# Kernel optimization log

Measured on AMD Instinct MI355X. Metric: run time of the kernel, lower is better.

Reference implementation:

```python
import jax, jax.numpy as jnp
import numpy as np

N, E, IN, OUT, EF = 20000, 100000, 32, 32, 16
NEG = -1e30  # finite sentinel for masked scores (avoids inf*0 grads)


def setup_inputs() -> dict:
    key = jax.random.key(0)
    ks = jax.random.split(key, 8)
    return {
        "feat": jax.random.normal(ks[0], (N, IN), jnp.float32),
        "efeat": jax.random.normal(ks[1], (E, EF), jnp.float32),
        "src": jax.random.randint(ks[2], (E,), 0, N, dtype=jnp.int32),
        "dst": jax.random.randint(ks[3], (E,), 0, N, dtype=jnp.int32),
        "etype": jax.random.randint(ks[4], (E,), 0, 2, dtype=jnp.int32),
        "attn_w": jax.random.normal(ks[5], (2 * IN, 1), jnp.float32) * 0.1,
        "attn_b": jnp.zeros((1,), jnp.float32),
        "ef1_w": jax.random.normal(ks[6], (EF, IN * OUT), jnp.float32) * 0.05,
        "ef1_b": jnp.zeros((IN * OUT,), jnp.float32),
        "ef2_w": jax.random.normal(ks[7], (EF, IN * OUT), jnp.float32) * 0.05,
        "ef2_b": jnp.zeros((IN * OUT,), jnp.float32),
        "bias": jnp.zeros((OUT,), jnp.float32),
    }


def reference(feat, efeat, src, dst, etype, attn_w, attn_b,
              ef1_w, ef1_b, ef2_w, ef2_b, bias):
    n_nodes = feat.shape[0]
    z_src = feat[src]                      # [E, IN] gather src features
    z_dst = feat[dst]                      # [E, IN] gather dst features
    # per-edge scalar attention score: leaky_relu(Linear(cat(z_src, z_dst)))
    score = jax.nn.leaky_relu(
        (jnp.concatenate([z_src, z_dst], axis=1) @ attn_w + attn_b)[:, 0]
    )  # [E]

    def relation_agg(mask, w, b):
        # edge-specific weight matrices: [E, IN, OUT]
        We = (efeat @ w + b).reshape(E, IN, OUT)
        # message per edge = src_feat @ W_e  (sum over IN commutes with attn)
        msg = jnp.einsum('ei,eio->eo', z_src, We)        # [E, OUT]
        # segment softmax over incoming edges of this relation per dst node
        s = jnp.where(mask, score, NEG)
        smax = jax.ops.segment_max(s, dst, num_segments=n_nodes)
        ex = jnp.where(mask, jnp.exp(s - smax[dst]), 0.0)
        den = jax.ops.segment_sum(ex, dst, num_segments=n_nodes)
        alpha = ex / jnp.where(den > 0, den, 1.0)[dst]   # [E]
        # attention-weighted scatter-sum to dst nodes
        return jax.ops.segment_sum(alpha[:, None] * msg, dst,
                                   num_segments=n_nodes)  # [N, OUT]

    rst = relation_agg(etype == 0, ef1_w, ef1_b) \
        + relation_agg(etype == 1, ef2_w, ef2_b) \
        + bias
    return rst
```

## Files before the change

kernel.cpp:

```cpp
#include <hip/hip_runtime.h>

typedef __attribute__((ext_vector_type(8))) short bf16x8;
typedef __attribute__((ext_vector_type(16))) float f32x16;

__device__ __forceinline__ unsigned short f2b(float x) {
    unsigned u = __float_as_uint(x);
    unsigned r = (u + 0x7fffu + ((u >> 16) & 1u)) >> 16;
    return (unsigned short)r;
}

__global__ void k_init(const float* __restrict__ feat, const float* __restrict__ attn_w,
                       const int* __restrict__ dst, const int* __restrict__ etype,
                       const float* __restrict__ w1, const float* __restrict__ b1,
                       const float* __restrict__ w2, const float* __restrict__ b2,
                       float* __restrict__ ps, float* __restrict__ pd,
                       unsigned short* __restrict__ PA, int* __restrict__ hist,
                       int E, int N) {
    int idx = blockIdx.x * blockDim.x + threadIdx.x;
    if (idx < N) {
        const float4* zp = (const float4*)(feat + (long)idx * 32);
        const float4* aw = (const float4*)attn_w;
        float a = 0.f, b = 0.f;
        #pragma unroll
        for (int j = 0; j < 8; ++j) {
            float4 z = zp[j], wa = aw[j], wb = aw[8 + j];
            a = fmaf(z.x, wa.x, a); a = fmaf(z.y, wa.y, a);
            a = fmaf(z.z, wa.z, a); a = fmaf(z.w, wa.w, a);
            b = fmaf(z.x, wb.x, b); b = fmaf(z.y, wb.y, b);
            b = fmaf(z.z, wb.z, b); b = fmaf(z.w, wb.w, b);
        }
        ps[idx] = a; pd[idx] = b;
    }
    if (idx < 2 * 17 * 2 * 64) {
        int l = idx & 63;
        int x = idx >> 6;
        int h = x & 1; x >>= 1;
        int t = x % 17;
        int r = x / 17;
        const float* W = r ? w2 : w1;
        const float* B = r ? b2 : b1;
        int o = l & 31;
        int kb = h * 16 + (l >> 5) * 8;
        unsigned short v[8];
        #pragma unroll
        for (int j = 0; j < 8; ++j) {
            int i = kb + j;
            float s = (t < 16) ? W[t * 1024 + i * 32 + o] : B[i * 32 + o];
            v[j] = f2b(s);
        }
        uint4 pack;
        pack.x = (unsigned)v[0] | ((unsigned)v[1] << 16);
        pack.y = (unsigned)v[2] | ((unsigned)v[3] << 16);
        pack.z = (unsigned)v[4] | ((unsigned)v[5] << 16);
        pack.w = (unsigned)v[6] | ((unsigned)v[7] << 16);
        *((uint4*)PA + idx) = pack;
    }
    if (idx < E) atomicAdd(&hist[etype[idx] * N + dst[idx]], 1);
}

__global__ __launch_bounds__(256) void k_scan1(const int* __restrict__ hist,
                                               int* __restrict__ rowptr,
                                               int* __restrict__ bsum, int n) {
    __shared__ int s[256];
    int t = threadIdx.x;
    int i0 = blockIdx.x * 1024 + t * 4;
    int h[4];
    #pragma unroll
    for (int j = 0; j < 4; ++j) h[j] = (i0 + j < n) ? hist[i0 + j] : 0;
    int tot = h[0] + h[1] + h[2] + h[3];
    s[t] = tot;
    __syncthreads();
    for (int d = 1; d < 256; d <<= 1) {
        int x = (t >= d) ? s[t - d] : 0;
        __syncthreads();
        s[t] += x;
        __syncthreads();
    }
    int excl = s[t] - tot;
    int run = excl;
    #pragma unroll
    for (int j = 0; j < 4; ++j) {
        if (i0 + j < n) rowptr[i0 + j] = run;
        run += h[j];
    }
    if (t == 255) bsum[blockIdx.x] = s[255];
}

__global__ void k_scan2(int* __restrict__ bsum, int nb) {
    int lane = threadIdx.x & 63;
    int carry = 0;
    for (int c = 0; c < nb; c += 64) {
        int i = c + lane;
        int v = (i < nb) ? bsum[i] : 0;
        int inc = v;
        #pragma unroll
        for (int d = 1; d < 64; d <<= 1) {
            int x = __shfl_up(inc, d);
            if (lane >= d) inc += x;
        }
        if (i < nb) bsum[i] = inc - v + carry;
        carry += __shfl(inc, 63);
    }
}

__global__ void k_scan3(int* __restrict__ rowptr, const int* __restrict__ bsum,
                        int* __restrict__ cursor, int n, int E) {
    int i = blockIdx.x * blockDim.x + threadIdx.x;
    if (i < n) {
        int v = rowptr[i] + bsum[i >> 10];
        rowptr[i] = v;
        cursor[i] = v;
    }
    if (i == 0) rowptr[n] = E;
}

__global__ void k_score(const int* __restrict__ src, const int* __restrict__ dst,
                        const int* __restrict__ etype,
                        const float* __restrict__ ps, const float* __restrict__ pd,
                        const float* __restrict__ attn_b,
                        int* __restrict__ cursor, int* __restrict__ sortidx,
                        float* __restrict__ exs, int E, int N) {
    int e = blockIdx.x * blockDim.x + threadIdx.x;
    if (e >= E) return;
    int d = dst[e];
    float sc = ps[src[e]] + pd[d] + attn_b[0];
    sc = sc >= 0.f ? sc : 0.01f * sc;
    float v = __expf(sc);
    int key = etype[e] * N + d;
    int pos = atomicAdd(&cursor[key], 1);
    sortidx[pos] = e;
    exs[pos] = v;
}

__global__ __launch_bounds__(256) void k_msg(
    const float* __restrict__ feat, const float* __restrict__ efeat,
    const int* __restrict__ src, const unsigned short* __restrict__ PA,
    const int* __restrict__ sortidx, const int* __restrict__ rowptr,
    float* __restrict__ wmsg, int E, int N) {
    int r = blockIdx.y;
    int cnt0 = rowptr[N];
    int relstart = r ? cnt0 : 0;
    int count = r ? (E - cnt0) : cnt0;
    int base = blockIdx.x * 128;
    if (count <= 0 || base >= count) return;

    __shared__ __align__(16) char smem[18432];
    unsigned short (*z_bf)[32] = (unsigned short(*)[32])smem;
    float (*ut)[128] = (float(*)[128])(smem + 8192);
    float (*msgl)[36] = (float(*)[36])smem;

    int tid = threadIdx.x;
    {
        int el = tid >> 1, half = tid & 1;
        int gi = base + el;
        int e = sortidx[relstart + min(gi, count - 1)];
        int s = src[e];
        const float4* zp = (const float4*)(feat + (long)s * 32 + half * 16);
        float4 a0 = zp[0], a1 = zp[1], a2 = zp[2], a3 = zp[3];
        unsigned short* zd = &z_bf[el][half * 16];
        zd[0] = f2b(a0.x); zd[1] = f2b(a0.y); zd[2]  = f2b(a0.z); zd[3]  = f2b(a0.w);
        zd[4] = f2b(a1.x); zd[5] = f2b(a1.y); zd[6]  = f2b(a1.z); zd[7]  = f2b(a1.w);
        zd[8] = f2b(a2.x); zd[9] = f2b(a2.y); zd[10] = f2b(a2.z); zd[11] = f2b(a2.w);
        zd[12] = f2b(a3.x); zd[13] = f2b(a3.y); zd[14] = f2b(a3.z); zd[15] = f2b(a3.w);
        const float4* up = (const float4*)(efeat + (long)e * 16 + half * 8);
        float4 c0 = up[0], c1 = up[1];
        int fb = half * 8;
        ut[fb + 0][el] = c0.x; ut[fb + 1][el] = c0.y;
        ut[fb + 2][el] = c0.z; ut[fb + 3][el] = c0.w;
        ut[fb + 4][el] = c1.x; ut[fb + 5][el] = c1.y;
        ut[fb + 6][el] = c1.z; ut[fb + 7][el] = c1.w;
    }
    __syncthreads();

    int lane = tid & 63;
    int ecol = (tid >> 6) * 32 + (lane & 31);
    int kb = (lane >> 5) * 8;
    bf16x8 b0 = *(const bf16x8*)&z_bf[ecol][kb];
    bf16x8 b1 = *(const bf16x8*)&z_bf[ecol][16 + kb];

    const bf16x8* pa = (const bf16x8*)PA + (long)r * 34 * 64 + lane;

    f32x16 msg;
    {
        bf16x8 a0 = pa[32 * 64];
        bf16x8 a1 = pa[33 * 64];
        f32x16 c;
        #pragma unroll
        for (int k = 0; k < 16; ++k) c[k] = 0.f;
        c = __builtin_amdgcn_mfma_f32_32x32x16_bf16(a0, b0, c, 0, 0, 0);
        c = __builtin_amdgcn_mfma_f32_32x32x16_bf16(a1, b1, c, 0, 0, 0);
        msg = c;
    }
    float uu[16];
    #pragma unroll
    for (int t = 0; t < 16; ++t) uu[t] = ut[t][ecol];
    #pragma unroll 4
    for (int t = 0; t < 16; ++t) {
        bf16x8 a0 = pa[(t * 2 + 0) * 64];
        bf16x8 a1 = pa[(t * 2 + 1) * 64];
        f32x16 c;
        #pragma unroll
        for (int k = 0; k < 16; ++k) c[k] = 0.f;
        c = __builtin_amdgcn_mfma_f32_32x32x16_bf16(a0, b0, c, 0, 0, 0);
        c = __builtin_amdgcn_mfma_f32_32x32x16_bf16(a1, b1, c, 0, 0, 0);
        #pragma unroll
        for (int k = 0; k < 16; ++k) msg[k] = fmaf(uu[t], c[k], msg[k]);
    }
    __syncthreads();

    {
        int ob = 4 * (lane >> 5);
        #pragma unroll
        for (int k = 0; k < 16; ++k)
            msgl[ecol][ob + (k & 3) + 8 * (k >> 2)] = msg[k];
    }
    __syncthreads();

    {
        float4* wb = (float4*)(wmsg + (long)(relstart + base) * 32);
        #pragma unroll
        for (int j = 0; j < 4; ++j) {
            int flat = j * 256 + tid;
            int row = flat >> 3, col = (flat & 7) * 4;
            if (base + row < count)
                wb[flat] = *(const float4*)&msgl[row][col];
        }
    }
}

__global__ void k_reduce(const int* __restrict__ rowptr, const float* __restrict__ exs,
                         const float* __restrict__ wmsg, const float* __restrict__ bias,
                         float* __restrict__ out, int N) {
    int tid = blockIdx.x * blockDim.x + threadIdx.x;
    if (tid >= N * 8) return;
    int n = tid >> 3, og = tid & 7;
    float4 acc = ((const float4*)bias)[og];
    #pragma unroll 1
    for (int r = 0; r < 2; ++r) {
        int k = r * N + n;
        int s = rowptr[k], e2 = rowptr[k + 1];
        if (s >= e2) continue;
        float den = 0.f;
        #pragma unroll 1
        for (int p = s; p < e2; ++p) den += exs[p];
        float inv = 1.f / den;
        #pragma unroll 1
        for (int p = s; p < e2; ++p) {
            float w = exs[p] * inv;
            float4 m = *(const float4*)(wmsg + (long)p * 32 + og * 4);
            acc.x = fmaf(w, m.x, acc.x); acc.y = fmaf(w, m.y, acc.y);
            acc.z = fmaf(w, m.z, acc.z); acc.w = fmaf(w, m.w, acc.w);
        }
    }
    ((float4*)out)[tid] = acc;
}

extern "C" void kernel_launch(void* const* d_in, const int* in_sizes, int n_in,
                              void* d_out, int out_size, void* d_ws, size_t ws_size,
                              hipStream_t stream) {
    const float* feat   = (const float*)d_in[0];
    const float* efeat  = (const float*)d_in[1];
    const int*   src    = (const int*)d_in[2];
    const int*   dst    = (const int*)d_in[3];
    const int*   etype  = (const int*)d_in[4];
    const float* attn_w = (const float*)d_in[5];
    const float* attn_b = (const float*)d_in[6];
    const float* ef1_w  = (const float*)d_in[7];
    const float* ef1_b  = (const float*)d_in[8];
    const float* ef2_w  = (const float*)d_in[9];
    const float* ef2_b  = (const float*)d_in[10];
    const float* bias   = (const float*)d_in[11];

    int E = in_sizes[2];
    int N = in_sizes[0] / 32;
    int n2 = 2 * N;

    float*          ps      = (float*)d_ws;
    float*          pd      = ps + N;
    unsigned short* PA      = (unsigned short*)(pd + N);
    int*            hist    = (int*)(PA + 2 * 17 * 2 * 64 * 8);
    int*            rowptr  = hist + n2;
    int*            cursor  = rowptr + n2 + 1;
    int*            bsum    = cursor + n2;
    int*            sortidx = bsum + 64;
    float*          exs     = (float*)(sortidx + E);
    float*          wmsg    = (float*)(((size_t)(exs + E) + 15) & ~(size_t)15);
    float*          out     = (float*)d_out;

    int nb = (n2 + 1023) / 1024;

    hipMemsetAsync(hist, 0, (size_t)n2 * sizeof(int), stream);
    k_init<<<(E + 255) / 256, 256, 0, stream>>>(feat, attn_w, dst, etype,
                                                ef1_w, ef1_b, ef2_w, ef2_b,
                                                ps, pd, PA, hist, E, N);
    k_scan1<<<nb, 256, 0, stream>>>(hist, rowptr, bsum, n2);
    k_scan2<<<1, 64, 0, stream>>>(bsum, nb);
    k_scan3<<<(n2 + 255) / 256, 256, 0, stream>>>(rowptr, bsum, cursor, n2, E);
    k_score<<<(E + 255) / 256, 256, 0, stream>>>(src, dst, etype, ps, pd, attn_b,
                                                 cursor, sortidx, exs, E, N);
    dim3 mgrid((E + 127) / 128, 2);
    k_msg<<<mgrid, 256, 0, stream>>>(feat, efeat, src, PA, sortidx, rowptr,
                                     wmsg, E, N);
    k_reduce<<<(N * 8 + 255) / 256, 256, 0, stream>>>(rowptr, exs, wmsg, bias, out, N);
}
```

Baseline: 54.31 us.

## Fuse preprocessing kernels into one cooperative kernel and store messages in bf16

Replaces the memset plus five small preprocessing kernels (init, three scan passes, score/bucket) with one cooperative kernel using grid-wide syncs, cutting launch overhead and inter-kernel gaps. It also stores per-edge weighted messages in bf16 instead of fp32, halving the write and read traffic between the message and reduce kernels. Costs are grid-sync overhead, a fixed 256-block grid that may underuse the GPU for edge loops, and extra rounding of messages to bf16. The single-block bsum scan now assumes nb is at most 64.

```diff
diff --git a/kernel.cpp b/kernel.cpp
--- a/kernel.cpp
+++ b/kernel.cpp
@@ -1,4 +1,7 @@
 #include <hip/hip_runtime.h>
+#include <hip/hip_cooperative_groups.h>
+
+namespace cg = cooperative_groups;
 
 typedef __attribute__((ext_vector_type(8))) short bf16x8;
 typedef __attribute__((ext_vector_type(16))) float f32x16;
@@ -8,17 +11,34 @@
     unsigned r = (u + 0x7fffu + ((u >> 16) & 1u)) >> 16;
     return (unsigned short)r;
 }
-
-__global__ void k_init(const float* __restrict__ feat, const float* __restrict__ attn_w,
-                       const int* __restrict__ dst, const int* __restrict__ etype,
-                       const float* __restrict__ w1, const float* __restrict__ b1,
-                       const float* __restrict__ w2, const float* __restrict__ b2,
-                       float* __restrict__ ps, float* __restrict__ pd,
-                       unsigned short* __restrict__ PA, int* __restrict__ hist,
-                       int E, int N) {
-    int idx = blockIdx.x * blockDim.x + threadIdx.x;
-    if (idx < N) {
-        const float4* zp = (const float4*)(feat + (long)idx * 32);
+__device__ __forceinline__ float b2f(unsigned short u) {
+    return __uint_as_float((unsigned)u << 16);
+}
+
+__global__ __launch_bounds__(256) void k_pre(
+    const float* __restrict__ feat, const float* __restrict__ attn_w,
+    const float* __restrict__ attn_b,
+    const int* __restrict__ src, const int* __restrict__ dst,
+    const int* __restrict__ etype,
+    const float* __restrict__ w1, const float* __restrict__ b1,
+    const float* __restrict__ w2, const float* __restrict__ b2,
+    float* __restrict__ ps, float* __restrict__ pd,
+    unsigned short* __restrict__ PA, int* __restrict__ hist,
+    int* __restrict__ rowptr, int* __restrict__ cursor,
+    int* __restrict__ bsum, int* __restrict__ sortidx,
+    float* __restrict__ exs, int E, int N, int nb) {
+    cg::grid_group g = cg::this_grid();
+    __shared__ int s[256];
+    int tid = threadIdx.x, bid = blockIdx.x;
+    int gid = bid * 256 + tid;
+    int gtot = gridDim.x * 256;
+    int n2 = 2 * N;
+
+    for (int i = gid; i < n2; i += gtot) hist[i] = 0;
+    g.sync();
+
+    for (int i = gid; i < N; i += gtot) {
+        const float4* zp = (const float4*)(feat + (long)i * 32);
         const float4* aw = (const float4*)attn_w;
         float a = 0.f, b = 0.f;
         #pragma unroll
@@ -29,11 +49,11 @@
             b = fmaf(z.x, wb.x, b); b = fmaf(z.y, wb.y, b);
             b = fmaf(z.z, wb.z, b); b = fmaf(z.w, wb.w, b);
         }
-        ps[idx] = a; pd[idx] = b;
-    }
-    if (idx < 2 * 17 * 2 * 64) {
-        int l = idx & 63;
-        int x = idx >> 6;
+        ps[i] = a; pd[i] = b;
+    }
+    if (gid < 2 * 17 * 2 * 64) {
+        int l = gid & 63;
+        int x = gid >> 6;
         int h = x & 1; x >>= 1;
         int t = x % 17;
         int r = x / 17;
@@ -45,98 +65,82 @@
         #pragma unroll
         for (int j = 0; j < 8; ++j) {
             int i = kb + j;
-            float s = (t < 16) ? W[t * 1024 + i * 32 + o] : B[i * 32 + o];
-            v[j] = f2b(s);
+            float sv = (t < 16) ? W[t * 1024 + i * 32 + o] : B[i * 32 + o];
+            v[j] = f2b(sv);
         }
         uint4 pack;
         pack.x = (unsigned)v[0] | ((unsigned)v[1] << 16);
         pack.y = (unsigned)v[2] | ((unsigned)v[3] << 16);
         pack.z = (unsigned)v[4] | ((unsigned)v[5] << 16);
         pack.w = (unsigned)v[6] | ((unsigned)v[7] << 16);
-        *((uint4*)PA + idx) = pack;
-    }
-    if (idx < E) atomicAdd(&hist[etype[idx] * N + dst[idx]], 1);
-}
-
-__global__ __launch_bounds__(256) void k_scan1(const int* __restrict__ hist,
-                                               int* __restrict__ rowptr,
-                                               int* __restrict__ bsum, int n) {
-    __shared__ int s[256];
-    int t = threadIdx.x;
-    int i0 = blockIdx.x * 1024 + t * 4;
-    int h[4];
-    #pragma unroll
-    for (int j = 0; j < 4; ++j) h[j] = (i0 + j < n) ? hist[i0 + j] : 0;
-    int tot = h[0] + h[1] + h[2] + h[3];
-    s[t] = tot;
-    __syncthreads();
-    for (int d = 1; d < 256; d <<= 1) {
-        int x = (t >= d) ? s[t - d] : 0;
+        *((uint4*)PA + gid) = pack;
+    }
+    for (int e = gid; e < E; e += gtot)
+        atomicAdd(&hist[etype[e] * N + dst[e]], 1);
+    g.sync();
+
+    if (bid < nb) {
+        int i0 = bid * 1024 + tid * 4;
+        int h[4];
+        #pragma unroll
+        for (int j = 0; j < 4; ++j) h[j] = (i0 + j < n2) ? hist[i0 + j] : 0;
+        int tot = h[0] + h[1] + h[2] + h[3];
+        s[tid] = tot;
         __syncthreads();
-        s[t] += x;
-        __syncthreads();
-    }
-    int excl = s[t] - tot;
-    int run = excl;
-    #pragma unroll
-    for (int j = 0; j < 4; ++j) {
-        if (i0 + j < n) rowptr[i0 + j] = run;
-        run += h[j];
-    }
-    if (t == 255) bsum[blockIdx.x] = s[255];
-}
-
-__global__ void k_scan2(int* __restrict__ bsum, int nb) {
-    int lane = threadIdx.x & 63;
-    int carry = 0;
-    for (int c = 0; c < nb; c += 64) {
-        int i = c + lane;
-        int v = (i < nb) ? bsum[i] : 0;
+        for (int d = 1; d < 256; d <<= 1) {
+            int x = (tid >= d) ? s[tid - d] : 0;
+            __syncthreads();
+            s[tid] += x;
+            __syncthreads();
+        }
+        int run = s[tid] - tot;
+        #pragma unroll
+        for (int j = 0; j < 4; ++j) {
+            if (i0 + j < n2) rowptr[i0 + j] = run;
+            run += h[j];
+        }
+        if (tid == 255) bsum[bid] = s[255];
+    }
+    g.sync();
+
+    if (bid == 0 && tid < 64) {
+        int lane = tid;
+        int v = (lane < nb) ? bsum[lane] : 0;
         int inc = v;
         #pragma unroll
         for (int d = 1; d < 64; d <<= 1) {
             int x = __shfl_up(inc, d);
             if (lane >= d) inc += x;
         }
-        if (i < nb) bsum[i] = inc - v + carry;
-        carry += __shfl(inc, 63);
-    }
-}
-
-__global__ void k_scan3(int* __restrict__ rowptr, const int* __restrict__ bsum,
-                        int* __restrict__ cursor, int n, int E) {
-    int i = blockIdx.x * blockDim.x + threadIdx.x;
-    if (i < n) {
+        if (lane < nb) bsum[lane] = inc - v;
+    }
+    g.sync();
+
+    for (int i = gid; i < n2; i += gtot) {
         int v = rowptr[i] + bsum[i >> 10];
         rowptr[i] = v;
         cursor[i] = v;
     }
-    if (i == 0) rowptr[n] = E;
-}
-
-__global__ void k_score(const int* __restrict__ src, const int* __restrict__ dst,
-                        const int* __restrict__ etype,
-                        const float* __restrict__ ps, const float* __restrict__ pd,
-                        const float* __restrict__ attn_b,
-                        int* __restrict__ cursor, int* __restrict__ sortidx,
-                        float* __restrict__ exs, int E, int N) {
-    int e = blockIdx.x * blockDim.x + threadIdx.x;
-    if (e >= E) return;
-    int d = dst[e];
-    float sc = ps[src[e]] + pd[d] + attn_b[0];
-    sc = sc >= 0.f ? sc : 0.01f * sc;
-    float v = __expf(sc);
-    int key = etype[e] * N + d;
-    int pos = atomicAdd(&cursor[key], 1);
-    sortidx[pos] = e;
-    exs[pos] = v;
+    if (gid == 0) rowptr[n2] = E;
+    g.sync();
+
+    for (int e = gid; e < E; e += gtot) {
+        int d = dst[e];
+        float sc = ps[src[e]] + pd[d] + attn_b[0];
+        sc = sc >= 0.f ? sc : 0.01f * sc;
+        float v = __expf(sc);
+        int key = etype[e] * N + d;
+        int pos = atomicAdd(&cursor[key], 1);
+        sortidx[pos] = e;
+        exs[pos] = v;
+    }
 }
 
 __global__ __launch_bounds__(256) void k_msg(
     const float* __restrict__ feat, const float* __restrict__ efeat,
     const int* __restrict__ src, const unsigned short* __restrict__ PA,
     const int* __restrict__ sortidx, const int* __restrict__ rowptr,
-    float* __restrict__ wmsg, int E, int N) {
+    unsigned short* __restrict__ wmsg, int E, int N) {
     int r = blockIdx.y;
     int cnt0 = rowptr[N];
     int relstart = r ? cnt0 : 0;
@@ -154,8 +158,8 @@
         int el = tid >> 1, half = tid & 1;
         int gi = base + el;
         int e = sortidx[relstart + min(gi, count - 1)];
-        int s = src[e];
-        const float4* zp = (const float4*)(feat + (long)s * 32 + half * 16);
+        int sn = src[e];
+        const float4* zp = (const float4*)(feat + (long)sn * 32 + half * 16);
         float4 a0 = zp[0], a1 = zp[1], a2 = zp[2], a3 = zp[3];
         unsigned short* zd = &z_bf[el][half * 16];
         zd[0] = f2b(a0.x); zd[1] = f2b(a0.y); zd[2]  = f2b(a0.z); zd[3]  = f2b(a0.w);
@@ -217,19 +221,27 @@
     __syncthreads();
 
     {
-        float4* wb = (float4*)(wmsg + (long)(relstart + base) * 32);
-        #pragma unroll
-        for (int j = 0; j < 4; ++j) {
+        uint4* wb = (uint4*)(wmsg + (long)(relstart + base) * 32);
+        #pragma unroll
+        for (int j = 0; j < 2; ++j) {
             int flat = j * 256 + tid;
-            int row = flat >> 3, col = (flat & 7) * 4;
-            if (base + row < count)
-                wb[flat] = *(const float4*)&msgl[row][col];
+            int row = flat >> 2, col = (flat & 3) * 8;
+            if (base + row < count) {
+                const float* mr = &msgl[row][col];
+                uint4 pk;
+                pk.x = (unsigned)f2b(mr[0]) | ((unsigned)f2b(mr[1]) << 16);
+                pk.y = (unsigned)f2b(mr[2]) | ((unsigned)f2b(mr[3]) << 16);
+                pk.z = (unsigned)f2b(mr[4]) | ((unsigned)f2b(mr[5]) << 16);
+                pk.w = (unsigned)f2b(mr[6]) | ((unsigned)f2b(mr[7]) << 16);
+                wb[flat] = pk;
+            }
         }
     }
 }
 
 __global__ void k_reduce(const int* __restrict__ rowptr, const float* __restrict__ exs,
-                         const float* __restrict__ wmsg, const float* __restrict__ bias,
+                         const unsigned short* __restrict__ wmsg,
+                         const float* __restrict__ bias,
                          float* __restrict__ out, int N) {
     int tid = blockIdx.x * blockDim.x + threadIdx.x;
     if (tid >= N * 8) return;
@@ -247,9 +259,11 @@
         #pragma unroll 1
         for (int p = s; p < e2; ++p) {
             float w = exs[p] * inv;
-            float4 m = *(const float4*)(wmsg + (long)p * 32 + og * 4);
-            acc.x = fmaf(w, m.x, acc.x); acc.y = fmaf(w, m.y, acc.y);
-            acc.z = fmaf(w, m.z, acc.z); acc.w = fmaf(w, m.w, acc.w);
+            ushort4 m = *(const ushort4*)(wmsg + (long)p * 32 + og * 4);
+            acc.x = fmaf(w, b2f(m.x), acc.x);
+            acc.y = fmaf(w, b2f(m.y), acc.y);
+            acc.z = fmaf(w, b2f(m.z), acc.z);
+            acc.w = fmaf(w, b2f(m.w), acc.w);
         }
     }
     ((float4*)out)[tid] = acc;
@@ -274,6 +288,7 @@
     int E = in_sizes[2];
     int N = in_sizes[0] / 32;
     int n2 = 2 * N;
+    int nb = (n2 + 1023) / 1024;
 
     float*          ps      = (float*)d_ws;
     float*          pd      = ps + N;
@@ -284,20 +299,19 @@
     int*            bsum    = cursor + n2;
     int*            sortidx = bsum + 64;
     float*          exs     = (float*)(sortidx + E);
-    float*          wmsg    = (float*)(((size_t)(exs + E) + 15) & ~(size_t)15);
+    unsigned short* wmsg    = (unsigned short*)(((size_t)(exs + E) + 15) & ~(size_t)15);
     float*          out     = (float*)d_out;
 
-    int nb = (n2 + 1023) / 1024;
-
-    hipMemsetAsync(hist, 0, (size_t)n2 * sizeof(int), stream);
-    k_init<<<(E + 255) / 256, 256, 0, stream>>>(feat, attn_w, dst, etype,
-                                                ef1_w, ef1_b, ef2_w, ef2_b,
-                                                ps, pd, PA, hist, E, N);
-    k_scan1<<<nb, 256, 0, stream>>>(hist, rowptr, bsum, n2);
-    k_scan2<<<1, 64, 0, stream>>>(bsum, nb);
-    k_scan3<<<(n2 + 255) / 256, 256, 0, stream>>>(rowptr, bsum, cursor, n2, E);
-    k_score<<<(E + 255) / 256, 256, 0, stream>>>(src, dst, etype, ps, pd, attn_b,
-                                                 cursor, sortidx, exs, E, N);
+    void* args[] = {
+        (void*)&feat, (void*)&attn_w, (void*)&attn_b,
+        (void*)&src, (void*)&dst, (void*)&etype,
+        (void*)&ef1_w, (void*)&ef1_b, (void*)&ef2_w, (void*)&ef2_b,
+        (void*)&ps, (void*)&pd, (void*)&PA, (void*)&hist,
+        (void*)&rowptr, (void*)&cursor, (void*)&bsum, (void*)&sortidx,
+        (void*)&exs, (void*)&E, (void*)&N, (void*)&nb
+    };
+    hipLaunchCooperativeKernel((void*)k_pre, dim3(256), dim3(256), args, 0, stream);
+
     dim3 mgrid((E + 127) / 128, 2);
     k_msg<<<mgrid, 256, 0, stream>>>(feat, efeat, src, PA, sortidx, rowptr,
                                      wmsg, E, N);
```

New measurement: 186.4 us. 3.43x slower.
